# Kernel optimization log

Measured on AMD Instinct MI355X. Metric: run time of the kernel, lower is better.

Reference implementation:

```python
import jax, jax.numpy as jnp
import numpy as np

# ---- sRGB <-> CIELAB (D65) helpers, matching standard torch lab2rgb/rgb2lab ----
_RGB2XYZ = jnp.array([[0.412453, 0.357580, 0.180423],
                      [0.212671, 0.715160, 0.072169],
                      [0.019334, 0.119193, 0.950227]], dtype=jnp.float32)
_XYZ2RGB = jnp.array([[ 3.2404542, -1.5371385, -0.4985314],
                      [-0.9692660,  1.8760108,  0.0415560],
                      [ 0.0556434, -0.2040259,  1.0572252]], dtype=jnp.float32)
_WHITE = jnp.array([0.95047, 1.0, 1.08883], dtype=jnp.float32)
_EPS = 0.008856      # (6/29)^3
_KAPPA = 7.787

def _srgb_to_linear(c):
    safe = jnp.maximum(c, 0.04045)
    return jnp.where(c <= 0.04045, c / 12.92, ((safe + 0.055) / 1.055) ** 2.4)

def _linear_to_srgb(c):
    safe = jnp.maximum(c, 0.0031308)
    return jnp.where(c <= 0.0031308, 12.92 * c, 1.055 * safe ** (1.0 / 2.4) - 0.055)

def rgb2lab(rgb):
    lin = _srgb_to_linear(rgb)                      # [N,3]
    xyz = (lin @ _RGB2XYZ.T) / _WHITE               # [N,3]
    safe = jnp.maximum(xyz, _EPS)
    f = jnp.where(xyz > _EPS, jnp.cbrt(safe), _KAPPA * xyz + 16.0 / 116.0)
    fx, fy, fz = f[..., 0], f[..., 1], f[..., 2]
    L = 116.0 * fy - 16.0
    a = 500.0 * (fx - fy)
    b = 200.0 * (fy - fz)
    return jnp.stack([L, a, b], axis=-1)

def lab2rgb(lab):
    L, a, b = lab[..., 0], lab[..., 1], lab[..., 2]
    fy = (L + 16.0) / 116.0
    fx = fy + a / 500.0
    fz = fy - b / 200.0
    f = jnp.stack([fx, fy, fz], axis=-1)
    f3 = f ** 3
    t = jnp.where(f3 > _EPS, f3, (f - 16.0 / 116.0) / _KAPPA)
    xyz = t * _WHITE
    lin = xyz @ _XYZ2RGB.T
    return _linear_to_srgb(lin)

def _forward(x, w_seq1, b_seq1, w_seq2, b_seq2, w_lin, b_lin,
             w_comb, b_comb, w_logd, b_logd, w_final, b_final):
    # lab branch
    seq = jnp.tanh(x @ w_seq1 + b_seq1) @ w_seq2 + b_seq2        # [N,3]
    lin = x @ w_lin + b_lin                                      # [N,3]
    final_lab = jnp.concatenate([lin, seq], axis=-1) @ w_comb + b_comb
    # log-density branch
    x_rgb = lab2rgb(x)
    log_density = -jnp.log10(x_rgb)
    model_processed = log_density @ w_logd + b_logd
    back_to_lab = rgb2lab(10.0 ** model_processed)
    return jnp.concatenate([final_lab, back_to_lab], axis=-1) @ w_final + b_final


def setup_inputs() -> dict:
    key = jax.random.key(0)
    ks = jax.random.split(key, 13)
    N, H = 2_097_152, 64

    def lin_init(kw, kb, fan_in, fan_out):
        bound = 1.0 / np.sqrt(fan_in)
        w = jax.random.uniform(kw, (fan_in, fan_out), minval=-bound, maxval=bound, dtype=jnp.float32)
        b = jax.random.uniform(kb, (fan_out,), minval=-bound, maxval=bound, dtype=jnp.float32)
        return w, b

    # valid Lab inputs: sample sRGB away from 0/1 then convert
    rgb = jax.random.uniform(ks[0], (N, 3), minval=0.05, maxval=0.95, dtype=jnp.float32)
    x = rgb2lab(rgb)

    kk = jax.random.split(ks[1], 12)
    w_seq1, b_seq1 = lin_init(kk[0], kk[1], 3, H)
    w_seq2, b_seq2 = lin_init(kk[2], kk[3], H, 3)
    w_lin, b_lin = lin_init(kk[4], kk[5], 3, 3)
    w_comb, b_comb = lin_init(kk[6], kk[7], 6, 3)
    w_logd, b_logd = lin_init(kk[8], kk[9], 3, 3)
    w_final, b_final = lin_init(kk[10], kk[11], 6, 3)
    return {"x": x,
            "w_seq1": w_seq1, "b_seq1": b_seq1, "w_seq2": w_seq2, "b_seq2": b_seq2,
            "w_lin": w_lin, "b_lin": b_lin, "w_comb": w_comb, "b_comb": b_comb,
            "w_logd": w_logd, "b_logd": b_logd, "w_final": w_final, "b_final": b_final}


def reference(x, w_seq1, b_seq1, w_seq2, b_seq2, w_lin, b_lin,
              w_comb, b_comb, w_logd, b_logd, w_final, b_final):
    return _forward(x, w_seq1, b_seq1, w_seq2, b_seq2, w_lin, b_lin,
                    w_comb, b_comb, w_logd, b_logd, w_final, b_final)
```

## Files before the change

### kernel.cpp

```cpp
#include <hip/hip_runtime.h>

__device__ __forceinline__ float fexp2(float x) { return __builtin_amdgcn_exp2f(x); }
__device__ __forceinline__ float flog2(float x) { return __builtin_amdgcn_logf(x); }
__device__ __forceinline__ float frcp (float x) { return __builtin_amdgcn_rcpf(x); }
__device__ __forceinline__ float ffma (float a, float b, float c) { return __builtin_fmaf(a, b, c); }

#define LAB_EPS   0.008856f
#define F16_116   0.13793103448275862f
#define INV_KAPPA 0.12841915central

__global__ __launch_bounds__(256) void fused_kernel(
    const float* __restrict__ x,
    const float* __restrict__ w_seq1, const float* __restrict__ b_seq1,
    const float* __restrict__ w_seq2, const float* __restrict__ b_seq2,
    const float* __restrict__ w_lin,  const float* __restrict__ b_lin,
    const float* __restrict__ w_comb, const float* __restrict__ b_comb,
    const float* __restrict__ w_logd, const float* __restrict__ b_logd,
    const float* __restrict__ w_final,const float* __restrict__ b_final,
    float* __restrict__ out, int n)
{
    __shared__ float4 wlds[128];
    __shared__ float  smlds[33];

    const int tid = threadIdx.x;
    if (tid < 64) {
        const int j = tid;
        float H3[9];
        for (int i = 0; i < 3; ++i)
            for (int c = 0; c < 3; ++c) {
                float h = 0.f;
                for (int m = 0; m < 3; ++m) h += w_comb[(i + 3) * 3 + m] * w_final[m * 3 + c];
                H3[i * 3 + c] = h;
            }
        const float w0 = w_seq2[j * 3 + 0], w1 = w_seq2[j * 3 + 1], w2 = w_seq2[j * 3 + 2];
        wlds[2 * j]     = make_float4(w_seq1[j], w_seq1[64 + j], w_seq1[128 + j], b_seq1[j]);
        wlds[2 * j + 1] = make_float4(w0 * H3[0] + w1 * H3[3] + w2 * H3[6],
                                      w0 * H3[1] + w1 * H3[4] + w2 * H3[7],
                                      w0 * H3[2] + w1 * H3[5] + w2 * H3[8], 0.f);
        if (j == 0) {
            float G[9];
            for (int i = 0; i < 3; ++i)
                for (int c = 0; c < 3; ++c) {
                    float gg = 0.f;
                    for (int m = 0; m < 3; ++m) gg += w_comb[i * 3 + m] * w_final[m * 3 + c];
                    G[i * 3 + c] = gg;
                }
            for (int k = 0; k < 3; ++k)
                for (int c = 0; c < 3; ++c) {
                    float s = 0.f;
                    for (int i = 0; i < 3; ++i) s += w_lin[k * 3 + i] * G[i * 3 + c];
                    smlds[k * 3 + c]      = s;
                    smlds[9  + k * 3 + c] = w_final[(k + 3) * 3 + c];
                    smlds[18 + k * 3 + c] = w_logd[k * 3 + c];
                }
            for (int c = 0; c < 3; ++c) {
                float s = b_final[c];
                for (int i = 0; i < 3; ++i)
                    s += b_lin[i] * G[i * 3 + c] + b_seq2[i] * H3[i * 3 + c]
                       + b_comb[i] * w_final[i * 3 + c];
                smlds[27 + c] = b_logd[c];
                smlds[30 + c] = s;
            }
        }
    }
    __syncthreads();

    float A[9], Wfb[9], Wld[9], bld[3], cv[3];
#pragma unroll
    for (int i = 0; i < 9; ++i) { A[i] = smlds[i]; Wfb[i] = smlds[9 + i]; Wld[i] = smlds[18 + i]; }
#pragma unroll
    for (int i = 0; i < 3; ++i) { bld[i] = smlds[27 + i]; cv[i] = smlds[30 + i]; }

    const int g = blockIdx.x * blockDim.x + tid;
    if (g * 8 >= n) return;

    const float4* xin = reinterpret_cast<const float4*>(x) + (size_t)g * 6;
    const float4 v0 = xin[0], v1 = xin[1], v2 = xin[2], v3 = xin[3], v4 = xin[4], v5 = xin[5];
    float xs[8][3] = {
        {v0.x, v0.y, v0.z}, {v0.w, v1.x, v1.y}, {v1.z, v1.w, v2.x}, {v2.y, v2.z, v2.w},
        {v3.x, v3.y, v3.z}, {v3.w, v4.x, v4.y}, {v4.z, v4.w, v5.x}, {v5.y, v5.z, v5.w}};

    float acc[8][3];
#pragma unroll
    for (int p = 0; p < 8; ++p) { acc[p][0] = 0.f; acc[p][1] = 0.f; acc[p][2] = 0.f; }

#pragma unroll 4
    for (int j = 0; j < 64; ++j) {
        const float4 wa = wlds[2 * j];
        const float4 wb = wlds[2 * j + 1];
#pragma unroll
        for (int p = 0; p < 8; ++p) {
            float t = ffma(xs[p][0], wa.x, ffma(xs[p][1], wa.y, ffma(xs[p][2], wa.z, wa.w)));
            float e = fexp2(t * 2.8853900817779268f);
            float r = frcp(e + 1.0f);
            float h = ffma(-2.0f, r, 1.0f);
            acc[p][0] = ffma(h, wb.x, acc[p][0]);
            acc[p][1] = ffma(h, wb.y, acc[p][1]);
            acc[p][2] = ffma(h, wb.z, acc[p][2]);
        }
    }

    float ov[24];
#pragma unroll
    for (int p = 0; p < 8; ++p) {
        const float L = xs[p][0], aa = xs[p][1], bb = xs[p][2];
        const float fy = (L + 16.0f) * (1.0f / 116.0f);
        const float fx = ffma(aa,  0.002f, fy);
        const float fz = ffma(bb, -0.005f, fy);
        float rgb[3];
        {
            const float f3x = fx * fx * fx, f3y = fy * fy * fy, f3z = fz * fz * fz;
            const float tx = f3x > LAB_EPS ? f3x : (fx - F16_116) * (1.0f / 7.787f);
            const float ty = f3y > LAB_EPS ? f3y : (fy - F16_116) * (1.0f / 7.787f);
            const float tz = f3z > LAB_EPS ? f3z : (fz - F16_116) * (1.0f / 7.787f);
            const float X = tx * 0.95047f, Y = ty, Z = tz * 1.08883f;
            const float linv[3] = {
                 3.2404542f * X - 1.5371385f * Y - 0.4985314f * Z,
                -0.9692660f * X + 1.8760108f * Y + 0.0415560f * Z,
                 0.0556434f * X - 0.2040259f * Y + 1.0572252f * Z};
#pragma unroll
            for (int c = 0; c < 3; ++c) {
                const float cc = linv[c];
                const float lo = 12.92f * cc;
                const float hi = ffma(1.055f,
                                      fexp2(flog2(fmaxf(cc, 0.0031308f)) * (1.0f / 2.4f)),
                                      -0.055f);
                rgb[c] = cc <= 0.0031308f ? lo : hi;
            }
        }
        const float ld0 = -0.30102999566398120f * flog2(rgb[0]);
        const float ld1 = -0.30102999566398120f * flog2(rgb[1]);
        const float ld2 = -0.30102999566398120f * flog2(rgb[2]);
        float lin2[3];
#pragma unroll
        for (int c = 0; c < 3; ++c) {
            const float mp  = ffma(ld0, Wld[c], ffma(ld1, Wld[3 + c], ffma(ld2, Wld[6 + c], bld[c])));
            const float r10 = fexp2(mp * 3.3219280948873623f);
            const float lo  = r10 * (1.0f / 12.92f);
            const float base = (fmaxf(r10, 0.04045f) + 0.055f) * (1.0f / 1.055f);
            const float hi  = fexp2(2.4f * flog2(base));
            lin2[c] = r10 <= 0.04045f ? lo : hi;
        }
        const float X2 = (0.412453f * lin2[0] + 0.357580f * lin2[1] + 0.180423f * lin2[2]) * (1.0f / 0.95047f);
        const float Y2 =  0.212671f * lin2[0] + 0.715160f * lin2[1] + 0.072169f * lin2[2];
        const float Z2 = (0.019334f * lin2[0] + 0.119193f * lin2[1] + 0.950227f * lin2[2]) * (1.0f / 1.08883f);
        const float fX = X2 > LAB_EPS ? fexp2(flog2(fmaxf(X2, LAB_EPS)) * (1.0f / 3.0f)) : ffma(7.787f, X2, F16_116);
        const float fY = Y2 > LAB_EPS ? fexp2(flog2(fmaxf(Y2, LAB_EPS)) * (1.0f / 3.0f)) : ffma(7.787f, Y2, F16_116);
        const float fZ = Z2 > LAB_EPS ? fexp2(flog2(fmaxf(Z2, LAB_EPS)) * (1.0f / 3.0f)) : ffma(7.787f, Z2, F16_116);
        const float bL = ffma(116.0f, fY, -16.0f);
        const float bA = 500.0f * (fX - fY);
        const float bB = 200.0f * (fY - fZ);
#pragma unroll
        for (int c = 0; c < 3; ++c) {
            float o = cv[c];
            o = ffma(L,  A[c],     o);
            o = ffma(aa, A[3 + c], o);
            o = ffma(bb, A[6 + c], o);
            o += acc[p][c];
            o = ffma(bL, Wfb[c],     o);
            o = ffma(bA, Wfb[3 + c], o);
            o = ffma(bB, Wfb[6 + c], o);
            ov[p * 3 + c] = o;
        }
    }

    float4* op = reinterpret_cast<float4*>(out) + (size_t)g * 6;
#pragma unroll
    for (int i = 0; i < 6; ++i)
        op[i] = make_float4(ov[4 * i], ov[4 * i + 1], ov[4 * i + 2], ov[4 * i + 3]);
}

extern "C" void kernel_launch(void* const* d_in, const int* in_sizes, int n_in,
                              void* d_out, int out_size, void* d_ws, size_t ws_size,
                              hipStream_t stream)
{
    const float* x       = (const float*)d_in[0];
    const float* w_seq1  = (const float*)d_in[1];
    const float* b_seq1  = (const float*)d_in[2];
    const float* w_seq2  = (const float*)d_in[3];
    const float* b_seq2  = (const float*)d_in[4];
    const float* w_lin   = (const float*)d_in[5];
    const float* b_lin   = (const float*)d_in[6];
    const float* w_comb  = (const float*)d_in[7];
    const float* b_comb  = (const float*)d_in[8];
    const float* w_logd  = (const float*)d_in[9];
    const float* b_logd  = (const float*)d_in[10];
    const float* w_final = (const float*)d_in[11];
    const float* b_final = (const float*)d_in[12];
    float* outp = (float*)d_out;

    const int n = in_sizes[0] / 3;
    const int threads = 256;
    const int total_threads = (n + 7) / 8;
    const int blocks = (total_threads + threads - 1) / threads;

    fused_kernel<<<blocks, threads, 0, stream>>>(
        x, w_seq1, b_seq1, w_seq2, b_seq2, w_lin, b_lin, w_comb, b_comb,
        w_logd, b_logd, w_final, b_final, outp, n);
}
```

Measured before the change: 150.9 us.

## Use packed FP32 FMA for tanh MLP and halve points per thread

The hidden-layer loop now works on pairs of points with packed v2f FMAs, so the dot products and output accumulation can map to packed FP32 instructions. The tanh scale constant is folded into the first-layer weights at load time, which removes one multiply per hidden unit. Each thread now handles 4 points instead of 8, doubling thread count and lowering register pressure. Exp and rcp remain scalar transcendentals, so those may still bound throughput, and per-thread LDS weight reads are now amortized over half as many points.

```diff
diff --git a/kernel.cpp b/kernel.cpp
--- a/kernel.cpp
+++ b/kernel.cpp
@@ -1,13 +1,17 @@
 #include <hip/hip_runtime.h>
+
+typedef float v2f __attribute__((ext_vector_type(2)));
 
 __device__ __forceinline__ float fexp2(float x) { return __builtin_amdgcn_exp2f(x); }
 __device__ __forceinline__ float flog2(float x) { return __builtin_amdgcn_logf(x); }
 __device__ __forceinline__ float frcp (float x) { return __builtin_amdgcn_rcpf(x); }
 __device__ __forceinline__ float ffma (float a, float b, float c) { return __builtin_fmaf(a, b, c); }
-
-#define LAB_EPS   0.008856f
-#define F16_116   0.13793103448275862f
-#define INV_KAPPA 0.12841915central
+__device__ __forceinline__ v2f  splat(float s) { v2f v; v.x = s; v.y = s; return v; }
+__device__ __forceinline__ v2f  pkfma(v2f a, v2f b, v2f c) { return __builtin_elementwise_fma(a, b, c); }
+
+#define LAB_EPS 0.008856f
+#define F16_116 0.13793103448275862f
+#define TANH_K  2.8853900817779268f
 
 __global__ __launch_bounds__(256) void fused_kernel(
     const float* __restrict__ x,
@@ -33,7 +37,8 @@
                 H3[i * 3 + c] = h;
             }
         const float w0 = w_seq2[j * 3 + 0], w1 = w_seq2[j * 3 + 1], w2 = w_seq2[j * 3 + 2];
-        wlds[2 * j]     = make_float4(w_seq1[j], w_seq1[64 + j], w_seq1[128 + j], b_seq1[j]);
+        wlds[2 * j]     = make_float4(w_seq1[j] * TANH_K, w_seq1[64 + j] * TANH_K,
+                                      w_seq1[128 + j] * TANH_K, b_seq1[j] * TANH_K);
         wlds[2 * j + 1] = make_float4(w0 * H3[0] + w1 * H3[3] + w2 * H3[6],
                                       w0 * H3[1] + w1 * H3[4] + w2 * H3[7],
                                       w0 * H3[2] + w1 * H3[5] + w2 * H3[8], 0.f);
@@ -65,45 +70,57 @@
     }
     __syncthreads();
 
-    float A[9], Wfb[9], Wld[9], bld[3], cv[3];
-#pragma unroll
-    for (int i = 0; i < 9; ++i) { A[i] = smlds[i]; Wfb[i] = smlds[9 + i]; Wld[i] = smlds[18 + i]; }
-#pragma unroll
-    for (int i = 0; i < 3; ++i) { bld[i] = smlds[27 + i]; cv[i] = smlds[30 + i]; }
-
     const int g = blockIdx.x * blockDim.x + tid;
-    if (g * 8 >= n) return;
-
-    const float4* xin = reinterpret_cast<const float4*>(x) + (size_t)g * 6;
-    const float4 v0 = xin[0], v1 = xin[1], v2 = xin[2], v3 = xin[3], v4 = xin[4], v5 = xin[5];
-    float xs[8][3] = {
-        {v0.x, v0.y, v0.z}, {v0.w, v1.x, v1.y}, {v1.z, v1.w, v2.x}, {v2.y, v2.z, v2.w},
-        {v3.x, v3.y, v3.z}, {v3.w, v4.x, v4.y}, {v4.z, v4.w, v5.x}, {v5.y, v5.z, v5.w}};
-
-    float acc[8][3];
-#pragma unroll
-    for (int p = 0; p < 8; ++p) { acc[p][0] = 0.f; acc[p][1] = 0.f; acc[p][2] = 0.f; }
+    if (g * 4 >= n) return;
+
+    const float4* xin = reinterpret_cast<const float4*>(x) + (size_t)g * 3;
+    const float4 v0 = xin[0], v1 = xin[1], v2 = xin[2];
+    const float f[12] = {v0.x, v0.y, v0.z, v0.w, v1.x, v1.y, v1.z, v1.w, v2.x, v2.y, v2.z, v2.w};
+
+    v2f xs2[2][3];
+#pragma unroll
+    for (int q = 0; q < 2; ++q)
+#pragma unroll
+        for (int c = 0; c < 3; ++c) { xs2[q][c].x = f[6 * q + c]; xs2[q][c].y = f[6 * q + 3 + c]; }
+
+    v2f acc2[2][3];
+#pragma unroll
+    for (int q = 0; q < 2; ++q)
+#pragma unroll
+        for (int c = 0; c < 3; ++c) acc2[q][c] = splat(0.f);
 
 #pragma unroll 4
     for (int j = 0; j < 64; ++j) {
         const float4 wa = wlds[2 * j];
         const float4 wb = wlds[2 * j + 1];
 #pragma unroll
-        for (int p = 0; p < 8; ++p) {
-            float t = ffma(xs[p][0], wa.x, ffma(xs[p][1], wa.y, ffma(xs[p][2], wa.z, wa.w)));
-            float e = fexp2(t * 2.8853900817779268f);
-            float r = frcp(e + 1.0f);
-            float h = ffma(-2.0f, r, 1.0f);
-            acc[p][0] = ffma(h, wb.x, acc[p][0]);
-            acc[p][1] = ffma(h, wb.y, acc[p][1]);
-            acc[p][2] = ffma(h, wb.z, acc[p][2]);
+        for (int q = 0; q < 2; ++q) {
+            v2f t = pkfma(xs2[q][0], splat(wa.x),
+                    pkfma(xs2[q][1], splat(wa.y),
+                    pkfma(xs2[q][2], splat(wa.z), splat(wa.w))));
+            v2f e; e.x = fexp2(t.x); e.y = fexp2(t.y);
+            v2f ep = e + splat(1.0f);
+            v2f r; r.x = frcp(ep.x); r.y = frcp(ep.y);
+            v2f h = pkfma(splat(-2.0f), r, splat(1.0f));
+            acc2[q][0] = pkfma(h, splat(wb.x), acc2[q][0]);
+            acc2[q][1] = pkfma(h, splat(wb.y), acc2[q][1]);
+            acc2[q][2] = pkfma(h, splat(wb.z), acc2[q][2]);
         }
     }
 
-    float ov[24];
-#pragma unroll
-    for (int p = 0; p < 8; ++p) {
-        const float L = xs[p][0], aa = xs[p][1], bb = xs[p][2];
+    float A[9], Wfb[9], Wld[9], bld[3], cv[3];
+#pragma unroll
+    for (int i = 0; i < 9; ++i) { A[i] = smlds[i]; Wfb[i] = smlds[9 + i]; Wld[i] = smlds[18 + i]; }
+#pragma unroll
+    for (int i = 0; i < 3; ++i) { bld[i] = smlds[27 + i]; cv[i] = smlds[30 + i]; }
+
+    float ov[12];
+#pragma unroll
+    for (int p = 0; p < 4; ++p) {
+        const float L  = f[3 * p + 0], aa = f[3 * p + 1], bb = f[3 * p + 2];
+        const float a0 = (p & 1) ? acc2[p >> 1][0].y : acc2[p >> 1][0].x;
+        const float a1 = (p & 1) ? acc2[p >> 1][1].y : acc2[p >> 1][1].x;
+        const float a2 = (p & 1) ? acc2[p >> 1][2].y : acc2[p >> 1][2].x;
         const float fy = (L + 16.0f) * (1.0f / 116.0f);
         const float fx = ffma(aa,  0.002f, fy);
         const float fz = ffma(bb, -0.005f, fy);
@@ -156,7 +173,7 @@
             o = ffma(L,  A[c],     o);
             o = ffma(aa, A[3 + c], o);
             o = ffma(bb, A[6 + c], o);
-            o += acc[p][c];
+            o += (c == 0 ? a0 : (c == 1 ? a1 : a2));
             o = ffma(bL, Wfb[c],     o);
             o = ffma(bA, Wfb[3 + c], o);
             o = ffma(bB, Wfb[6 + c], o);
@@ -164,9 +181,9 @@
         }
     }
 
-    float4* op = reinterpret_cast<float4*>(out) + (size_t)g * 6;
-#pragma unroll
-    for (int i = 0; i < 6; ++i)
+    float4* op = reinterpret_cast<float4*>(out) + (size_t)g * 3;
+#pragma unroll
+    for (int i = 0; i < 3; ++i)
         op[i] = make_float4(ov[4 * i], ov[4 * i + 1], ov[4 * i + 2], ov[4 * i + 3]);
 }
 
@@ -191,7 +208,7 @@
 
     const int n = in_sizes[0] / 3;
     const int threads = 256;
-    const int total_threads = (n + 7) / 8;
+    const int total_threads = (n + 3) / 4;
     const int blocks = (total_threads + threads - 1) / threads;
 
     fused_kernel<<<blocks, threads, 0, stream>>>(
```

After: 140.9 us. 1.07x faster.

## Replace tanh exp/rcp with shared-memory lookup table and fold Lab output weights

Applied to the files above, without the earlier changes.

The tanh in the hidden layer is replaced by a 2048-entry shared-memory table of tanh(s)/s, indexed by t squared, with the first-layer weights prescaled so the table index is cheap. This removes the transcendental exp and reciprocal per hidden unit. The Lab-to-output affine step is folded into the final weights. Points per thread drop from 8 to 4, doubling the thread count. The table uses a nearest-bin approximation with no interpolation, which loses accuracy, and every block must fill the table, which adds startup work and LDS traffic.

```diff
diff --git a/kernel.cpp b/kernel.cpp
--- a/kernel.cpp
+++ b/kernel.cpp
@@ -2,12 +2,12 @@
 
 __device__ __forceinline__ float fexp2(float x) { return __builtin_amdgcn_exp2f(x); }
 __device__ __forceinline__ float flog2(float x) { return __builtin_amdgcn_logf(x); }
-__device__ __forceinline__ float frcp (float x) { return __builtin_amdgcn_rcpf(x); }
 __device__ __forceinline__ float ffma (float a, float b, float c) { return __builtin_fmaf(a, b, c); }
 
-#define LAB_EPS   0.008856f
-#define F16_116   0.13793103448275862f
-#define INV_KAPPA 0.12841915central
+#define LAB_EPS 0.008856f
+#define F16_116 0.13793103448275862f
+#define TSCALE  11.3137085f
+#define TCLAMP  45.2547f
 
 __global__ __launch_bounds__(256) void fused_kernel(
     const float* __restrict__ x,
@@ -19,10 +19,17 @@
     const float* __restrict__ w_final,const float* __restrict__ b_final,
     float* __restrict__ out, int n)
 {
+    __shared__ float  gtab[2048];
     __shared__ float4 wlds[128];
     __shared__ float  smlds[33];
 
     const int tid = threadIdx.x;
+
+    for (int k = tid; k < 2048; k += 256) {
+        const float su = sqrtf((k + 0.5f) * (1.0f / 128.0f));
+        gtab[k] = tanhf(su) / (su * TSCALE);
+    }
+
     if (tid < 64) {
         const int j = tid;
         float H3[9];
@@ -33,12 +40,13 @@
                 H3[i * 3 + c] = h;
             }
         const float w0 = w_seq2[j * 3 + 0], w1 = w_seq2[j * 3 + 1], w2 = w_seq2[j * 3 + 2];
-        wlds[2 * j]     = make_float4(w_seq1[j], w_seq1[64 + j], w_seq1[128 + j], b_seq1[j]);
+        wlds[2 * j]     = make_float4(w_seq1[j] * TSCALE, w_seq1[64 + j] * TSCALE,
+                                      w_seq1[128 + j] * TSCALE, b_seq1[j] * TSCALE);
         wlds[2 * j + 1] = make_float4(w0 * H3[0] + w1 * H3[3] + w2 * H3[6],
                                       w0 * H3[1] + w1 * H3[4] + w2 * H3[7],
                                       w0 * H3[2] + w1 * H3[5] + w2 * H3[8], 0.f);
         if (j == 0) {
-            float G[9];
+            float G[9], Wfb[9];
             for (int i = 0; i < 3; ++i)
                 for (int c = 0; c < 3; ++c) {
                     float gg = 0.f;
@@ -49,12 +57,15 @@
                 for (int c = 0; c < 3; ++c) {
                     float s = 0.f;
                     for (int i = 0; i < 3; ++i) s += w_lin[k * 3 + i] * G[i * 3 + c];
-                    smlds[k * 3 + c]      = s;
-                    smlds[9  + k * 3 + c] = w_final[(k + 3) * 3 + c];
+                    smlds[k * 3 + c] = s;
+                    Wfb[k * 3 + c]   = w_final[(k + 3) * 3 + c];
                     smlds[18 + k * 3 + c] = w_logd[k * 3 + c];
                 }
             for (int c = 0; c < 3; ++c) {
-                float s = b_final[c];
+                smlds[9 + c]     = 500.0f * Wfb[3 + c];
+                smlds[9 + 3 + c] = 116.0f * Wfb[c] - 500.0f * Wfb[3 + c] + 200.0f * Wfb[6 + c];
+                smlds[9 + 6 + c] = -200.0f * Wfb[6 + c];
+                float s = b_final[c] - 16.0f * Wfb[c];
                 for (int i = 0; i < 3; ++i)
                     s += b_lin[i] * G[i * 3 + c] + b_seq2[i] * H3[i * 3 + c]
                        + b_comb[i] * w_final[i * 3 + c];
@@ -65,44 +76,44 @@
     }
     __syncthreads();
 
-    float A[9], Wfb[9], Wld[9], bld[3], cv[3];
-#pragma unroll
-    for (int i = 0; i < 9; ++i) { A[i] = smlds[i]; Wfb[i] = smlds[9 + i]; Wld[i] = smlds[18 + i]; }
-#pragma unroll
-    for (int i = 0; i < 3; ++i) { bld[i] = smlds[27 + i]; cv[i] = smlds[30 + i]; }
-
     const int g = blockIdx.x * blockDim.x + tid;
-    if (g * 8 >= n) return;
-
-    const float4* xin = reinterpret_cast<const float4*>(x) + (size_t)g * 6;
-    const float4 v0 = xin[0], v1 = xin[1], v2 = xin[2], v3 = xin[3], v4 = xin[4], v5 = xin[5];
-    float xs[8][3] = {
-        {v0.x, v0.y, v0.z}, {v0.w, v1.x, v1.y}, {v1.z, v1.w, v2.x}, {v2.y, v2.z, v2.w},
-        {v3.x, v3.y, v3.z}, {v3.w, v4.x, v4.y}, {v4.z, v4.w, v5.x}, {v5.y, v5.z, v5.w}};
-
-    float acc[8][3];
-#pragma unroll
-    for (int p = 0; p < 8; ++p) { acc[p][0] = 0.f; acc[p][1] = 0.f; acc[p][2] = 0.f; }
+    if (g * 4 >= n) return;
+
+    const float4* xin = reinterpret_cast<const float4*>(x) + (size_t)g * 3;
+    const float4 v0 = xin[0], v1 = xin[1], v2 = xin[2];
+    const float xs[4][3] = {{v0.x, v0.y, v0.z}, {v0.w, v1.x, v1.y},
+                            {v1.z, v1.w, v2.x}, {v2.y, v2.z, v2.w}};
+
+    float acc[4][3];
+#pragma unroll
+    for (int p = 0; p < 4; ++p) { acc[p][0] = 0.f; acc[p][1] = 0.f; acc[p][2] = 0.f; }
 
 #pragma unroll 4
     for (int j = 0; j < 64; ++j) {
         const float4 wa = wlds[2 * j];
         const float4 wb = wlds[2 * j + 1];
 #pragma unroll
-        for (int p = 0; p < 8; ++p) {
+        for (int p = 0; p < 4; ++p) {
             float t = ffma(xs[p][0], wa.x, ffma(xs[p][1], wa.y, ffma(xs[p][2], wa.z, wa.w)));
-            float e = fexp2(t * 2.8853900817779268f);
-            float r = frcp(e + 1.0f);
-            float h = ffma(-2.0f, r, 1.0f);
+            t = fminf(fmaxf(t, -TCLAMP), TCLAMP);
+            const float u = t * t;
+            const int idx = (int)u;
+            const float h = t * gtab[idx];
             acc[p][0] = ffma(h, wb.x, acc[p][0]);
             acc[p][1] = ffma(h, wb.y, acc[p][1]);
             acc[p][2] = ffma(h, wb.z, acc[p][2]);
         }
     }
 
-    float ov[24];
-#pragma unroll
-    for (int p = 0; p < 8; ++p) {
+    float A[9], U[9], Wld[9], bld[3], cv[3];
+#pragma unroll
+    for (int i = 0; i < 9; ++i) { A[i] = smlds[i]; U[i] = smlds[9 + i]; Wld[i] = smlds[18 + i]; }
+#pragma unroll
+    for (int i = 0; i < 3; ++i) { bld[i] = smlds[27 + i]; cv[i] = smlds[30 + i]; }
+
+    float ov[12];
+#pragma unroll
+    for (int p = 0; p < 4; ++p) {
         const float L = xs[p][0], aa = xs[p][1], bb = xs[p][2];
         const float fy = (L + 16.0f) * (1.0f / 116.0f);
         const float fx = ffma(aa,  0.002f, fy);
@@ -147,9 +158,6 @@
         const float fX = X2 > LAB_EPS ? fexp2(flog2(fmaxf(X2, LAB_EPS)) * (1.0f / 3.0f)) : ffma(7.787f, X2, F16_116);
         const float fY = Y2 > LAB_EPS ? fexp2(flog2(fmaxf(Y2, LAB_EPS)) * (1.0f / 3.0f)) : ffma(7.787f, Y2, F16_116);
         const float fZ = Z2 > LAB_EPS ? fexp2(flog2(fmaxf(Z2, LAB_EPS)) * (1.0f / 3.0f)) : ffma(7.787f, Z2, F16_116);
-        const float bL = ffma(116.0f, fY, -16.0f);
-        const float bA = 500.0f * (fX - fY);
-        const float bB = 200.0f * (fY - fZ);
 #pragma unroll
         for (int c = 0; c < 3; ++c) {
             float o = cv[c];
@@ -157,16 +165,16 @@
             o = ffma(aa, A[3 + c], o);
             o = ffma(bb, A[6 + c], o);
             o += acc[p][c];
-            o = ffma(bL, Wfb[c],     o);
-            o = ffma(bA, Wfb[3 + c], o);
-            o = ffma(bB, Wfb[6 + c], o);
+            o = ffma(fX, U[c],     o);
+            o = ffma(fY, U[3 + c], o);
+            o = ffma(fZ, U[6 + c], o);
             ov[p * 3 + c] = o;
         }
     }
 
-    float4* op = reinterpret_cast<float4*>(out) + (size_t)g * 6;
-#pragma unroll
-    for (int i = 0; i < 6; ++i)
+    float4* op = reinterpret_cast<float4*>(out) + (size_t)g * 3;
+#pragma unroll
+    for (int i = 0; i < 3; ++i)
         op[i] = make_float4(ov[4 * i], ov[4 * i + 1], ov[4 * i + 2], ov[4 * i + 3]);
 }
 
@@ -191,7 +199,7 @@
 
     const int n = in_sizes[0] / 3;
     const int threads = 256;
-    const int total_threads = (n + 7) / 8;
+    const int total_threads = (n + 3) / 4;
     const int blocks = (total_threads + threads - 1) / threads;
 
     fused_kernel<<<blocks, threads, 0, stream>>>(
```

Measured after the change: 141.1 us. 1.07x faster.
